# Performance work log

Hardware: AMD Instinct MI355X
Metric: run time of the kernel (lower is better)

The kernel has to match this reference:

```python
import jax, jax.numpy as jnp
import numpy as np

B, S, DM, TD, H, HD = 2, 2048, 1024, 1024, 16, 64


def setup_inputs() -> dict:
    key = jax.random.key(0)
    k1, k2, k3, k4 = jax.random.split(key, 4)
    query = jax.random.normal(k1, (B, S, DM), dtype=jnp.float32)
    # fused QKV projection weight (nn.Linear weight layout: [out, in]) and output proj
    W_in = jax.random.normal(k2, (3 * TD, DM), dtype=jnp.float32) * 0.02
    W_out = jax.random.normal(k3, (DM, TD), dtype=jnp.float32) * 0.02
    # standard RoPE tables, broadcastable against [B, H, S, HD]
    inv_freq = 1.0 / (10000.0 ** (jnp.arange(0, HD, 2, dtype=jnp.float32) / HD))
    t = jnp.arange(S, dtype=jnp.float32)
    freqs = jnp.outer(t, inv_freq)                      # [S, HD/2]
    emb = jnp.concatenate([freqs, freqs], axis=-1)      # [S, HD]
    sin_q = jnp.sin(emb)[None, None]                    # [1,1,S,HD]
    cos_q = jnp.cos(emb)[None, None]
    # padding mask over keys: first length[b] positions valid (>= S/2 so no NaN rows)
    lengths = jax.random.randint(k4, (B,), S // 2, S + 1)
    attn_mask = jnp.arange(S)[None, :] < lengths[:, None]  # [B, S] bool
    return {"query": query, "W_in": W_in, "W_out": W_out,
            "sin_q": sin_q, "cos_q": cos_q, "attn_mask": attn_mask}


def _rotate_half(x):
    x1, x2 = jnp.split(x, 2, axis=-1)
    return jnp.concatenate([-x2, x1], axis=-1)


def reference(query, W_in, W_out, sin_q, cos_q, attn_mask):
    # fused QKV projection (proj_in, bias=False)
    qkv = query @ W_in.T                                # [B, S, 3*TD]
    q, k, v = jnp.split(qkv, 3, axis=-1)
    to_heads = lambda x: x.reshape(B, S, H, HD).transpose(0, 2, 1, 3)  # [B,H,S,HD]
    q, k, v = to_heads(q), to_heads(k), to_heads(v)
    # RoPE (prefix = 0 since sin covers full sequence)
    q = q * cos_q + _rotate_half(q) * sin_q
    k = k * cos_q + _rotate_half(k) * sin_q
    # SDPA with padding-mask bias + causal mask
    scale = 1.0 / jnp.sqrt(jnp.float32(HD))
    scores = jnp.einsum('bhqd,bhkd->bhqk', q, k) * scale  # [B,H,S,S]
    causal = jnp.arange(S)[:, None] >= jnp.arange(S)[None, :]  # [S, S]
    mask = attn_mask[:, None, None, :] & causal[None, None]    # [B,1,S,S]
    scores = jnp.where(mask, scores, -jnp.inf)
    attn = jax.nn.softmax(scores, axis=-1)
    out = jnp.einsum('bhqk,bhkd->bhqd', attn, v)        # [B,H,S,HD]
    out = out.transpose(0, 2, 1, 3).reshape(B, S, TD)
    return out @ W_out.T                                 # [B, S, DM]
```

## Files before the change

### kernel.cpp

```cpp
#include <hip/hip_runtime.h>
#include <hip/hip_bf16.h>

#define B_ 2
#define S_ 2048
#define DM_ 1024
#define TD_ 1024
#define H_ 16
#define HD_ 64

using bf16 = __hip_bfloat16;
typedef __attribute__((ext_vector_type(8))) short s8v;
typedef __attribute__((ext_vector_type(4))) float f4v;

__device__ __forceinline__ f4v mfma_bf16(s8v a, s8v b, f4v c) {
    return __builtin_amdgcn_mfma_f32_16x16x32_bf16(a, b, c, 0, 0, 0);
}

__device__ __forceinline__ unsigned cvt_pk_bf16(float a, float b) {
    unsigned r;
    asm("v_cvt_pk_bf16_f32 %0, %1, %2" : "=v"(r) : "v"(a), "v"(b));
    return r;
}
__device__ __forceinline__ int2 pack4bf(float a, float b, float c, float d) {
    int2 r;
    r.x = (int)cvt_pk_bf16(a, b);
    r.y = (int)cvt_pk_bf16(c, d);
    return r;
}

__device__ __forceinline__ bool detect_f32(const unsigned int* __restrict__ cosw) {
    return (cosw[0] & 0xFFFFu) == 0u;
}

__device__ __forceinline__ void gload_lds16(const bf16* g, void* l) {
    __builtin_amdgcn_global_load_lds(
        (const __attribute__((address_space(1))) unsigned int*)(const void*)g,
        (__attribute__((address_space(3))) unsigned int*)l,
        16, 0, 0);
}

#define NQ_  (B_ * S_ * DM_)
#define NWI_ (3 * TD_ * DM_)
#define NWO_ (DM_ * TD_)
#define NCVT_BLOCKS ((NQ_ + NWI_ + NWO_) / 2048)

__global__ __launch_bounds__(256)
void prep_all(const void* __restrict__ q, const void* __restrict__ wi,
              const void* __restrict__ wo, bf16* __restrict__ dst,
              const void* __restrict__ mask, int* __restrict__ lengths,
              const unsigned int* __restrict__ cosw) {
    const int bid = blockIdx.x;
    if (bid < NCVT_BLOCKS) {
        const bool f32 = detect_f32(cosw);
        int i = (bid * 256 + threadIdx.x) * 8;
        const void* src; int off;
        if (i < NQ_)              { src = q;  off = i; }
        else if (i < NQ_ + NWI_)  { src = wi; off = i - NQ_; }
        else                      { src = wo; off = i - NQ_ - NWI_; }
        if (f32) {
            const float* p = (const float*)src + off;
            float4 x = *reinterpret_cast<const float4*>(p);
            float4 y = *reinterpret_cast<const float4*>(p + 4);
            union { unsigned u[4]; int4 v; } t;
            t.u[0] = cvt_pk_bf16(x.x, x.y);
            t.u[1] = cvt_pk_bf16(x.z, x.w);
            t.u[2] = cvt_pk_bf16(y.x, y.y);
            t.u[3] = cvt_pk_bf16(y.z, y.w);
            *reinterpret_cast<int4*>(dst + i) = t.v;
        } else {
            *reinterpret_cast<int4*>(dst + i) =
                *reinterpret_cast<const int4*>((const bf16*)src + off);
        }
        return;
    }
    int b = bid - NCVT_BLOCKS;
    unsigned int w0 = ((const unsigned int*)mask)[0];
    int enc;
    if (w0 == 1u) enc = 0;
    else if (w0 == 0x01010101u) enc = 1;
    else if (w0 == 0x3F803F80u) enc = 2;
    else enc = 3;
    int cnt = 0;
    for (int s = threadIdx.x; s < S_; s += 256) {
        int i = b * S_ + s;
        bool v;
        if (enc == 0)      v = ((const int*)mask)[i] != 0;
        else if (enc == 1) v = ((const unsigned char*)mask)[i] != 0;
        else if (enc == 2) v = ((const unsigned short*)mask)[i] != 0;
        else               v = ((const float*)mask)[i] != 0.f;
        cnt += v ? 1 : 0;
    }
    __shared__ int red[256];
    red[threadIdx.x] = cnt;
    __syncthreads();
    for (int off = 128; off > 0; off >>= 1) {
        if (threadIdx.x < off) red[threadIdx.x] += red[threadIdx.x + off];
        __syncthreads();
    }
    if (threadIdx.x == 0) lengths[b] = red[0];
}

__global__ __launch_bounds__(256)
void gemm_nt(const bf16* __restrict__ A, const bf16* __restrict__ Bm,
             void* __restrict__ C, int M, int N, int K,
             int c_dyn, const unsigned int* __restrict__ cosw) {
    __shared__ bf16 lds_a[128 * 64];
    __shared__ bf16 lds_b[128 * 64];

    const bool cf32 = c_dyn && detect_f32(cosw);

    const int t = threadIdx.x;
    const int wave = t >> 6, lane = t & 63;
    const int quad = lane >> 4, l16 = lane & 15;
    const int wm = wave >> 1, wn = wave & 1;
    const int m0 = blockIdx.y * 128, n0 = blockIdx.x * 128;
    const int wuni = __builtin_amdgcn_readfirstlane(wave);

    f4v acc[4][4];
    #pragma unroll
    for (int i = 0; i < 4; i++)
        #pragma unroll
        for (int j = 0; j < 4; j++)
            acc[i][j] = f4v{0.f, 0.f, 0.f, 0.f};

    for (int k0 = 0; k0 < K; k0 += 64) {
        __syncthreads();
        #pragma unroll
        for (int i = 0; i < 4; i++) {
            int ci = i * 256 + t;
            int row = ci >> 3;
            int csrc = (ci & 7) ^ (row & 7);
            gload_lds16(A + (size_t)(m0 + row) * K + k0 + csrc * 8,
                        (char*)lds_a + i * 4096 + wuni * 1024);
            gload_lds16(Bm + (size_t)(n0 + row) * K + k0 + csrc * 8,
                        (char*)lds_b + i * 4096 + wuni * 1024);
        }
        __syncthreads();

        #pragma unroll
        for (int kk = 0; kk < 2; kk++) {
            s8v afr[4], bfr[4];
            #pragma unroll
            for (int mb = 0; mb < 4; mb++) {
                int r = wm * 64 + mb * 16 + l16;
                int ch = (kk * 4 + quad) ^ (l16 & 7);
                afr[mb] = *reinterpret_cast<const s8v*>(&lds_a[r * 64 + ch * 8]);
            }
            #pragma unroll
            for (int nb = 0; nb < 4; nb++) {
                int r = wn * 64 + nb * 16 + l16;
                int ch = (kk * 4 + quad) ^ (l16 & 7);
                bfr[nb] = *reinterpret_cast<const s8v*>(&lds_b[r * 64 + ch * 8]);
            }
            #pragma unroll
            for (int mb = 0; mb < 4; mb++)
                #pragma unroll
                for (int nb = 0; nb < 4; nb++)
                    acc[mb][nb] = mfma_bf16(bfr[nb], afr[mb], acc[mb][nb]);
        }
    }

    #pragma unroll
    for (int mb = 0; mb < 4; mb++) {
        int m = m0 + wm * 64 + mb * 16 + l16;
        #pragma unroll
        for (int nb = 0; nb < 4; nb++) {
            int n = n0 + wn * 64 + nb * 16 + quad * 4;
            f4v v = acc[mb][nb];
            if (cf32) {
                *reinterpret_cast<f4v*>(&((float*)C)[(size_t)m * N + n]) = v;
            } else {
                *reinterpret_cast<int2*>(&((bf16*)C)[(size_t)m * N + n]) =
                    pack4bf(v[0], v[1], v[2], v[3]);
            }
        }
    }
}

__global__ __launch_bounds__(256, 3)
void gemm_qkv(const bf16* __restrict__ A, const bf16* __restrict__ Bm,
              bf16* __restrict__ Qh, bf16* __restrict__ Kt, bf16* __restrict__ Vt,
              const void* __restrict__ sin_t, const void* __restrict__ cos_t) {
    __shared__ bf16 lds_a[128 * 64];
    __shared__ bf16 lds_b[128 * 64];

    const int t = threadIdx.x;
    const int wave = t >> 6, lane = t & 63;
    const int quad = lane >> 4, l16 = lane & 15;
    const int wm = wave >> 1, wn = wave & 1;
    const int m0 = blockIdx.y * 128, n0 = blockIdx.x * 128;
    const int wuni = __builtin_amdgcn_readfirstlane(wave);

    f4v acc[4][4];
    #pragma unroll
    for (int i = 0; i < 4; i++)
        #pragma unroll
        for (int j = 0; j < 4; j++)
            acc[i][j] = f4v{0.f, 0.f, 0.f, 0.f};

    for (int k0 = 0; k0 < 1024; k0 += 64) {
        __syncthreads();
        #pragma unroll
        for (int i = 0; i < 4; i++) {
            int ci = i * 256 + t;
            int row = ci >> 3;
            int csrc = (ci & 7) ^ (row & 7);
            gload_lds16(A + (size_t)(m0 + row) * 1024 + k0 + csrc * 8,
                        (char*)lds_a + i * 4096 + wuni * 1024);
            gload_lds16(Bm + (size_t)(n0 + row) * 1024 + k0 + csrc * 8,
                        (char*)lds_b + i * 4096 + wuni * 1024);
        }
        __syncthreads();

        #pragma unroll
        for (int kk = 0; kk < 2; kk++) {
            s8v afr[4], bfr[4];
            #pragma unroll
            for (int mb = 0; mb < 4; mb++) {
                int r = wm * 64 + mb * 16 + l16;
                int ch = (kk * 4 + quad) ^ (l16 & 7);
                afr[mb] = *reinterpret_cast<const s8v*>(&lds_a[r * 64 + ch * 8]);
            }
            #pragma unroll
            for (int nb = 0; nb < 4; nb++) {
                int r = wn * 64 + nb * 16 + l16;
                int ch = (kk * 4 + quad) ^ (l16 & 7);
                bfr[nb] = *reinterpret_cast<const s8v*>(&lds_b[r * 64 + ch * 8]);
            }
            #pragma unroll
            for (int mb = 0; mb < 4; mb++)
                #pragma unroll
                for (int nb = 0; nb < 4; nb++)
                    acc[mb][nb] = mfma_bf16(bfr[nb], afr[mb], acc[mb][nb]);
        }
    }

    const int region = n0 >> 10;
    if (region < 2) {
        const bool f32 = detect_f32((const unsigned int*)cos_t);
        #pragma unroll
        for (int mb = 0; mb < 4; mb++) {
            const int m = m0 + wm * 64 + mb * 16 + l16;
            const int b = m >> 11, s = m & 2047;
            #pragma unroll
            for (int nb = 0; nb < 4; nb++) {
                const int n = n0 + wn * 64 + nb * 16 + quad * 4;
                const int d = n & 63;
                const int h = (n >> 6) & 15;
                const float sgn = (nb < 2) ? -1.f : 1.f;
                f4v v  = acc[mb][nb];
                f4v vp = acc[mb][nb ^ 2];
                float cs[4], sn[4];
                if (f32) {
                    float4 c4 = *reinterpret_cast<const float4*>(
                        (const float*)cos_t + s * 64 + d);
                    float4 s4 = *reinterpret_cast<const float4*>(
                        (const float*)sin_t + s * 64 + d);
                    cs[0] = c4.x; cs[1] = c4.y; cs[2] = c4.z; cs[3] = c4.w;
                    sn[0] = s4.x; sn[1] = s4.y; sn[2] = s4.z; sn[3] = s4.w;
                } else {
                    const bf16* cp = (const bf16*)cos_t + s * 64 + d;
                    const bf16* sp = (const bf16*)sin_t + s * 64 + d;
                    #pragma unroll
                    for (int r = 0; r < 4; r++) {
                        cs[r] = __bfloat162float(cp[r]);
                        sn[r] = __bfloat162float(sp[r]);
                    }
                }
                float y[4];
                #pragma unroll
                for (int r = 0; r < 4; r++)
                    y[r] = v[r] * cs[r] + sgn * vp[r] * sn[r];
                if (region == 0) {
                    size_t o = ((size_t)(b * H_ + h) * S_ + s) * 64 + d;
                    *reinterpret_cast<int2*>(&Qh[o]) =
                        pack4bf(y[0] * 0.180336880f, y[1] * 0.180336880f,
                                y[2] * 0.180336880f, y[3] * 0.180336880f);
                } else {
                    size_t kt = ((size_t)(b * H_ + h) * 32 + (s >> 6)) * 4096;
                    int dp = ((((d >> 3) ^ (s & 7)) << 3) | (d & 7));
                    *reinterpret_cast<int2*>(&Kt[kt + (s & 63) * 64 + dp]) =
                        pack4bf(y[0], y[1], y[2], y[3]);
                }
            }
        }
    } else {
        __syncthreads();
        bf16* half_w = (wm == 0) ? lds_a : lds_b;
        #pragma unroll
        for (int mb = 0; mb < 4; mb++) {
            const int slr = mb * 16 + l16;
            #pragma unroll
            for (int nb = 0; nb < 4; nb++) {
                const int nl = wn * 64 + nb * 16 + quad * 4;
                f4v v = acc[mb][nb];
                int off = (((nl >> 3) ^ (slr & 7)) << 3) | (nl & 7);
                *reinterpret_cast<int2*>(&half_w[slr * 128 + off]) =
                    pack4bf(v[0], v[1], v[2], v[3]);
            }
        }
        __syncthreads();
        const int b  = m0 >> 11;
        const int h0 = (n0 - 2048) >> 6;
        const int r0 = t & 7;
        #pragma unroll
        for (int i = 0; i < 8; i++) {
            int id  = i * 256 + t;
            int kc  = id & 7;
            int d   = (id >> 3) & 63;
            int sbl = (id >> 9) & 1;
            int hh  = id >> 10;
            int cb  = (hh << 3) | (d >> 3);
            const short* half_r = reinterpret_cast<const short*>(
                sbl ? lds_b : lds_a);
            union { short s_[8]; int4 v4; } u;
            #pragma unroll
            for (int j = 0; j < 8; j++) {
                int e   = (j + r0) & 7;
                int slr = kc * 8 + e;
                u.s_[e] = half_r[slr * 128 + (((cb ^ e) << 3) | (d & 7))];
            }
            size_t tb = ((size_t)(b * H_ + h0 + hh) * 32 +
                         ((m0 & 2047) >> 6) + sbl) * 4096;
            *reinterpret_cast<int4*>(&Vt[tb + d * 64 + ((kc ^ (d & 7)) << 3)]) = u.v4;
        }
    }
}

__global__ __launch_bounds__(256)
void attn_fused(const bf16* __restrict__ Qh, const bf16* __restrict__ Kt,
                const bf16* __restrict__ Vt, const int* __restrict__ lengths,
                bf16* __restrict__ out) {
    __shared__ bf16 k_buf[2 * 4096];
    __shared__ bf16 v_buf[2 * 4096];
    __shared__ bf16 lds_p[4 * 16 * 72];

    const int t = threadIdx.x, wave = t >> 6, lane = t & 63;
    const int quad = lane >> 4, l16 = lane & 15;
    const int bid = blockIdx.x;
    const int slot = bid >> 3;
    const int bh = (bid & 7) * 4 + (slot >> 4);
    const int p = slot & 15;
    const int b = bh >> 4, h = bh & 15;

    const size_t hb = (size_t)bh * S_ * 64;
    const bf16* Ktp = Kt + (size_t)bh * 32 * 4096;
    const bf16* Vtp = Vt + (size_t)bh * 32 * 4096;
    const int wuni = __builtin_amdgcn_readfirstlane(wave);
    int len_raw = lengths[b];
    const int len_b = len_raw < 1 ? 1 : (len_raw > S_ ? S_ : len_raw);
    const int nkt_len = (len_b + 63) >> 6;

    #pragma unroll
    for (int pass = 0; pass < 2; pass++) {
        const int qb = pass ? (31 - p) : p;
        const int qbase = qb * 64;
        const int qrow_g = qbase + wave * 16 + l16;
        const int kmax = (qrow_g < len_b - 1) ? qrow_g : (len_b - 1);

        s8v qf[2];
        {
            const bf16* qptr = Qh + hb + (size_t)qrow_g * 64 + quad * 8;
            qf[0] = *reinterpret_cast<const s8v*>(qptr);
            qf[1] = *reinterpret_cast<const s8v*>(qptr + 32);
        }

        f4v o_acc[4];
        #pragma unroll
        for (int a = 0; a < 4; a++) o_acc[a] = f4v{0.f, 0.f, 0.f, 0.f};
        float l_sum = 0.f;

        const int nkt = (qb + 1) < nkt_len ? (qb + 1) : nkt_len;

        f4v s_prev[4];
        auto process_tile = [&](int pt, const bf16* vb) {
            const int pbase = pt * 64;
            const bool tail = (pt == qb) || (pbase + 64 > len_b);
            #pragma unroll
            for (int a = 0; a < 4; a++) {
                float e0[4];
                #pragma unroll
                for (int r = 0; r < 4; r++) {
                    float e = __builtin_amdgcn_exp2f(s_prev[a][r]);
                    if (tail) {
                        int key = pbase + a * 16 + quad * 4 + r;
                        e = (key <= kmax) ? e : 0.f;
                    }
                    e0[r] = e;
                    l_sum += e;
                }
                *reinterpret_cast<int2*>(
                    &lds_p[(wave * 16 + l16) * 72 + a * 16 + quad * 4]) =
                    pack4bf(e0[0], e0[1], e0[2], e0[3]);
            }
            asm volatile("s_waitcnt lgkmcnt(0)" ::: "memory");
            #pragma unroll
            for (int kk = 0; kk < 2; kk++) {
                s8v pf = *reinterpret_cast<const s8v*>(
                    &lds_p[(wave * 16 + l16) * 72 + kk * 32 + quad * 8]);
                #pragma unroll
                for (int a = 0; a < 4; a++) {
                    int ch = (kk * 4 + quad) ^ (l16 & 7);
                    s8v vf = *reinterpret_cast<const s8v*>(
                        &vb[(a * 16 + l16) * 64 + ch * 8]);
                    o_acc[a] = mfma_bf16(vf, pf, o_acc[a]);
                }
            }
        };

        #pragma unroll
        for (int i = 0; i < 2; i++) {
            int ci = i * 256 + t;
            gload_lds16(Ktp + ci * 8, (char*)k_buf + i * 4096 + wuni * 1024);
        }
        __syncthreads();

        for (int kt = 0; kt < nkt; kt++) {
            const int cur = kt & 1;
            {
                const bf16* vst = Vtp + (size_t)kt * 4096;
                #pragma unroll
                for (int i = 0; i < 2; i++) {
                    int ci = i * 256 + t;
                    gload_lds16(vst + ci * 8,
                                (char*)v_buf + cur * 8192 + i * 4096 + wuni * 1024);
                }
            }
            if (kt + 1 < nkt) {
                const bf16* kst = Ktp + (size_t)(kt + 1) * 4096;
                #pragma unroll
                for (int i = 0; i < 2; i++) {
                    int ci = i * 256 + t;
                    gload_lds16(kst + ci * 8,
                                (char*)k_buf + (cur ^ 1) * 8192 + i * 4096 + wuni * 1024);
                }
            }

            const bf16* kb = k_buf + cur * 4096;
            f4v s_acc[4];
            #pragma unroll
            for (int a = 0; a < 4; a++) s_acc[a] = f4v{0.f, 0.f, 0.f, 0.f};
            #pragma unroll
            for (int kk = 0; kk < 2; kk++) {
                #pragma unroll
                for (int a = 0; a < 4; a++) {
                    int ch = (kk * 4 + quad) ^ (l16 & 7);
                    s8v kf = *reinterpret_cast<const s8v*>(
                        &kb[(a * 16 + l16) * 64 + ch * 8]);
                    s_acc[a] = mfma_bf16(kf, qf[kk], s_acc[a]);
                }
            }

            if (kt > 0) process_tile(kt - 1, v_buf + ((kt - 1) & 1) * 4096);

            #pragma unroll
            for (int a = 0; a < 4; a++) s_prev[a] = s_acc[a];

            __syncthreads();
        }
        process_tile(nkt - 1, v_buf + ((nkt - 1) & 1) * 4096);

        l_sum += __shfl_xor(l_sum, 16);
        l_sum += __shfl_xor(l_sum, 32);
        float inv_l = 1.f / l_sum;
        size_t orow = ((size_t)(b * S_ + qrow_g)) * TD_ + h * 64;
        #pragma unroll
        for (int a = 0; a < 4; a++) {
            *reinterpret_cast<int2*>(&out[orow + a * 16 + quad * 4]) =
                pack4bf(o_acc[a][0] * inv_l, o_acc[a][1] * inv_l,
                        o_acc[a][2] * inv_l, o_acc[a][3] * inv_l);
        }
    }
}

extern "C" void kernel_launch(void* const* d_in, const int* in_sizes, int n_in,
                              void* d_out, int out_size, void* d_ws, size_t ws_size,
                              hipStream_t stream) {
    const void* query = d_in[0];
    const void* W_in  = d_in[1];
    const void* W_out = d_in[2];
    const void* sin_q = d_in[3];
    const void* cos_q = d_in[4];
    const void* mask  = d_in[5];
    const unsigned int* cosw = (const unsigned int*)cos_q;

    const size_t nQ  = NQ_;
    const size_t nWi = NWI_;
    const size_t nWo = NWO_;

    bf16* base = (bf16*)d_ws;
    bf16* attn = base;
    bf16* Vt   = base + (size_t)4096 * 1024;
    bf16* Qh   = base + (size_t)2 * 4096 * 1024;
    bf16* Kt   = Qh + nQ;
    bf16* qbf  = Kt + nQ;
    bf16* wibf = qbf + nQ;
    bf16* wobf = wibf + nWi;
    int* lengths = (int*)(wobf + nWo);

    prep_all<<<NCVT_BLOCKS + B_, 256, 0, stream>>>(
        query, W_in, W_out, qbf, mask, lengths, cosw);

    dim3 g1(3072 / 128, 4096 / 128);
    gemm_qkv<<<g1, 256, 0, stream>>>(qbf, wibf, Qh, Kt, Vt, sin_q, cos_q);

    attn_fused<<<512, 256, 0, stream>>>(Qh, Kt, Vt, lengths, attn);

    dim3 g2(1024 / 128, 4096 / 128);
    gemm_nt<<<g2, 256, 0, stream>>>(attn, wobf, d_out, 4096, 1024, 1024, 1, cosw);
}
```

Measured before the change: 192.6 us.

## Remap GEMM blocks for XCD-aware L2 reuse, shrink output tile, prioritize attention MFMA

Both GEMMs now use a 1D grid and a block-index remap so that blocks sharing the same M rows land on the same XCD (bid & 7), which is meant to improve L2 reuse of the A matrix. The output-projection GEMM drops its N tile from 128 to 64, so it launches 512 blocks instead of 256 and declares a higher occupancy bound, to fill all CUs. The attention kernel raises wave priority around its MFMA sections with s_setprio so the matrix work is issued ahead of softmax work from other waves. The smaller output tile lowers per-block reuse and adds more A-matrix reloads.

```diff
diff --git a/kernel.cpp b/kernel.cpp
--- a/kernel.cpp
+++ b/kernel.cpp
@@ -100,12 +100,12 @@
     if (threadIdx.x == 0) lengths[b] = red[0];
 }
 
-__global__ __launch_bounds__(256)
-void gemm_nt(const bf16* __restrict__ A, const bf16* __restrict__ Bm,
-             void* __restrict__ C, int M, int N, int K,
-             int c_dyn, const unsigned int* __restrict__ cosw) {
+__global__ __launch_bounds__(256, 4)
+void gemm_out(const bf16* __restrict__ A, const bf16* __restrict__ Bm,
+              void* __restrict__ C, int M, int N, int K,
+              int c_dyn, const unsigned int* __restrict__ cosw) {
     __shared__ bf16 lds_a[128 * 64];
-    __shared__ bf16 lds_b[128 * 64];
+    __shared__ bf16 lds_b[64 * 64];
 
     const bool cf32 = c_dyn && detect_f32(cosw);
 
@@ -113,14 +113,17 @@
     const int wave = t >> 6, lane = t & 63;
     const int quad = lane >> 4, l16 = lane & 15;
     const int wm = wave >> 1, wn = wave & 1;
-    const int m0 = blockIdx.y * 128, n0 = blockIdx.x * 128;
+    const int bid = blockIdx.x;
+    const int c = bid & 7, g = bid >> 3;
+    const int m0 = (c * 4 + (g & 3)) * 128;
+    const int n0 = (g >> 2) * 64;
     const int wuni = __builtin_amdgcn_readfirstlane(wave);
 
-    f4v acc[4][4];
+    f4v acc[4][2];
     #pragma unroll
     for (int i = 0; i < 4; i++)
         #pragma unroll
-        for (int j = 0; j < 4; j++)
+        for (int j = 0; j < 2; j++)
             acc[i][j] = f4v{0.f, 0.f, 0.f, 0.f};
 
     for (int k0 = 0; k0 < K; k0 += 64) {
@@ -132,6 +135,12 @@
             int csrc = (ci & 7) ^ (row & 7);
             gload_lds16(A + (size_t)(m0 + row) * K + k0 + csrc * 8,
                         (char*)lds_a + i * 4096 + wuni * 1024);
+        }
+        #pragma unroll
+        for (int i = 0; i < 2; i++) {
+            int ci = i * 256 + t;
+            int row = ci >> 3;
+            int csrc = (ci & 7) ^ (row & 7);
             gload_lds16(Bm + (size_t)(n0 + row) * K + k0 + csrc * 8,
                         (char*)lds_b + i * 4096 + wuni * 1024);
         }
@@ -139,7 +148,7 @@
 
         #pragma unroll
         for (int kk = 0; kk < 2; kk++) {
-            s8v afr[4], bfr[4];
+            s8v afr[4], bfr[2];
             #pragma unroll
             for (int mb = 0; mb < 4; mb++) {
                 int r = wm * 64 + mb * 16 + l16;
@@ -147,15 +156,15 @@
                 afr[mb] = *reinterpret_cast<const s8v*>(&lds_a[r * 64 + ch * 8]);
             }
             #pragma unroll
-            for (int nb = 0; nb < 4; nb++) {
-                int r = wn * 64 + nb * 16 + l16;
+            for (int nb = 0; nb < 2; nb++) {
+                int r = wn * 32 + nb * 16 + l16;
                 int ch = (kk * 4 + quad) ^ (l16 & 7);
                 bfr[nb] = *reinterpret_cast<const s8v*>(&lds_b[r * 64 + ch * 8]);
             }
             #pragma unroll
             for (int mb = 0; mb < 4; mb++)
                 #pragma unroll
-                for (int nb = 0; nb < 4; nb++)
+                for (int nb = 0; nb < 2; nb++)
                     acc[mb][nb] = mfma_bf16(bfr[nb], afr[mb], acc[mb][nb]);
         }
     }
@@ -164,8 +173,8 @@
     for (int mb = 0; mb < 4; mb++) {
         int m = m0 + wm * 64 + mb * 16 + l16;
         #pragma unroll
-        for (int nb = 0; nb < 4; nb++) {
-            int n = n0 + wn * 64 + nb * 16 + quad * 4;
+        for (int nb = 0; nb < 2; nb++) {
+            int n = n0 + wn * 32 + nb * 16 + quad * 4;
             f4v v = acc[mb][nb];
             if (cf32) {
                 *reinterpret_cast<f4v*>(&((float*)C)[(size_t)m * N + n]) = v;
@@ -188,7 +197,10 @@
     const int wave = t >> 6, lane = t & 63;
     const int quad = lane >> 4, l16 = lane & 15;
     const int wm = wave >> 1, wn = wave & 1;
-    const int m0 = blockIdx.y * 128, n0 = blockIdx.x * 128;
+    const int bid = blockIdx.x;
+    const int c = bid & 7, g = bid >> 3;
+    const int m0 = (c * 4 + (g & 3)) * 128;
+    const int n0 = (g >> 2) * 128;
     const int wuni = __builtin_amdgcn_readfirstlane(wave);
 
     f4v acc[4][4];
@@ -394,6 +406,7 @@
                     pack4bf(e0[0], e0[1], e0[2], e0[3]);
             }
             asm volatile("s_waitcnt lgkmcnt(0)" ::: "memory");
+            __builtin_amdgcn_s_setprio(1);
             #pragma unroll
             for (int kk = 0; kk < 2; kk++) {
                 s8v pf = *reinterpret_cast<const s8v*>(
@@ -406,6 +419,7 @@
                     o_acc[a] = mfma_bf16(vf, pf, o_acc[a]);
                 }
             }
+            __builtin_amdgcn_s_setprio(0);
         };
 
         #pragma unroll
@@ -440,6 +454,7 @@
             f4v s_acc[4];
             #pragma unroll
             for (int a = 0; a < 4; a++) s_acc[a] = f4v{0.f, 0.f, 0.f, 0.f};
+            __builtin_amdgcn_s_setprio(1);
             #pragma unroll
             for (int kk = 0; kk < 2; kk++) {
                 #pragma unroll
@@ -450,6 +465,7 @@
                     s_acc[a] = mfma_bf16(kf, qf[kk], s_acc[a]);
                 }
             }
+            __builtin_amdgcn_s_setprio(0);
 
             if (kt > 0) process_tile(kt - 1, v_buf + ((kt - 1) & 1) * 4096);
 
@@ -501,11 +517,9 @@
     prep_all<<<NCVT_BLOCKS + B_, 256, 0, stream>>>(
         query, W_in, W_out, qbf, mask, lengths, cosw);
 
-    dim3 g1(3072 / 128, 4096 / 128);
-    gemm_qkv<<<g1, 256, 0, stream>>>(qbf, wibf, Qh, Kt, Vt, sin_q, cos_q);
+    gemm_qkv<<<768, 256, 0, stream>>>(qbf, wibf, Qh, Kt, Vt, sin_q, cos_q);
 
     attn_fused<<<512, 256, 0, stream>>>(Qh, Kt, Vt, lengths, attn);
 
-    dim3 g2(1024 / 128, 4096 / 128);
-    gemm_nt<<<g2, 256, 0, stream>>>(attn, wobf, d_out, 4096, 1024, 1024, 1, cosw);
-}
+    gemm_out<<<512, 256, 0, stream>>>(attn, wobf, d_out, 4096, 1024, 1024, 1, cosw);
+}
```

Measured after the change: 177.2 us. 8.0% less time.
